# Kernel optimization log

Measured on AMD Instinct MI355X. Metric: run time of the kernel, lower is better.

The kernel has to match this reference:

```python
import jax, jax.numpy as jnp
import numpy as np

N, E, C1, E2, C2, B = 30000, 400000, 15000, 100000, 7500, 16
FV, FE, NC = 6, 3, 10


def _lin(k, i, o):
    kw, kb = jax.random.split(k)
    s = 1.0 / np.sqrt(i)
    w = jax.random.uniform(kw, (i, o), jnp.float32, -s, s)
    b = jax.random.uniform(kb, (o,), jnp.float32, -s, s)
    return w, b


def setup_inputs() -> dict:
    key = jax.random.key(0)
    ks = jax.random.split(key, 20)
    inp = {}
    inp["x"] = jax.random.normal(ks[0], (N, FV), jnp.float32)
    inp["edge_attr"] = jax.random.uniform(ks[1], (E, FE), jnp.float32)
    inp["pos"] = jax.random.uniform(ks[2], (N, 3), jnp.float32)
    inp["edge_index"] = jax.random.randint(ks[3], (2, E), 0, N)
    inp["batch"] = jnp.sort(jax.random.randint(ks[4], (N,), 0, B))
    inp["cluster1"] = jax.random.randint(ks[5], (N,), 0, C1)
    inp["edge_index2"] = jax.random.randint(ks[6], (2, E2), 0, C1)
    inp["cluster2"] = jax.random.randint(ks[7], (C1,), 0, C2)
    inp["w1a"], inp["b1a"] = _lin(ks[8], FE, 25)
    inp["w1b"], inp["b1b"] = _lin(ks[9], 25, 32 * FV)
    inp["root1"] = jax.random.normal(ks[10], (FV, 32), jnp.float32) / np.sqrt(FV)
    inp["bias1"] = jnp.zeros((32,), jnp.float32)
    inp["w2a"], inp["b2a"] = _lin(ks[11], 3, 25)
    inp["w2b"], inp["b2b"] = _lin(ks[12], 25, 32 * 64)
    inp["root2"] = jax.random.normal(ks[13], (32, 64), jnp.float32) / np.sqrt(32)
    inp["bias2"] = jnp.zeros((64,), jnp.float32)
    inp["fc1_w"], inp["fc1_b"] = _lin(ks[14], 64, 128)
    inp["fc2_w"], inp["fc2_b"] = _lin(ks[15], 128, NC)
    return inp


def _seg_mean(v, idx, n):
    s = jax.ops.segment_sum(v, idx, num_segments=n)
    c = jax.ops.segment_sum(jnp.ones(idx.shape, v.dtype), idx, num_segments=n)
    return s / jnp.maximum(c, 1.0)[:, None]


def _seg_max(v, idx, n):
    m = jax.ops.segment_max(v, idx, num_segments=n)
    return jnp.where(jnp.isfinite(m), m, 0.0)  # empty clusters -> 0


def _nnconv(x, src, dst, ea, wa, ba, wb, bb, root, bias, n, ci, co):
    # per-edge weight matrix from edge MLP: [E, ci, co]
    W = (jax.nn.relu(ea @ wa + ba) @ wb + bb).reshape(-1, ci, co)
    msg = jnp.einsum('ei,eio->eo', x[src], W)  # gather + per-edge matmul
    return _seg_mean(msg, dst, n) + x @ root + bias  # scatter-mean + root


def _cartesian(pos, src, dst):
    cart = pos[src] - pos[dst]
    return cart / (2.0 * jnp.max(jnp.abs(cart))) + 0.5  # T.Cartesian(norm=True)


def reference(x, edge_attr, pos, w1a, b1a, w1b, b1b, root1, bias1,
              w2a, b2a, w2b, b2b, root2, bias2, fc1_w, fc1_b, fc2_w, fc2_b,
              edge_index, batch, cluster1, edge_index2, cluster2):
    src1, dst1 = edge_index[0], edge_index[1]
    x1 = jax.nn.elu(_nnconv(x, src1, dst1, edge_attr, w1a, b1a, w1b, b1b,
                            root1, bias1, N, FV, 32))
    # max_pool with precomputed graclus cluster assignment
    xp = _seg_max(x1, cluster1, C1)
    posp = _seg_mean(pos, cluster1, C1)
    batchp = jnp.maximum(jax.ops.segment_max(batch, cluster1, num_segments=C1), 0)
    src2, dst2 = edge_index2[0], edge_index2[1]
    ea2 = _cartesian(posp, src2, dst2)
    x2 = jax.nn.elu(_nnconv(xp, src2, dst2, ea2, w2a, b2a, w2b, b2b,
                            root2, bias2, C1, 32, 64))
    # max_pool_x with second cluster assignment
    x3 = _seg_max(x2, cluster2, C2)
    batch2 = jnp.maximum(jax.ops.segment_max(batchp, cluster2, num_segments=C2), 0)
    g = _seg_mean(x3, batch2, B)  # global mean pool -> [B, 64]
    h = jax.nn.elu(g @ fc1_w + fc1_b)
    # dropout is identity in eval mode
    return jax.nn.log_softmax(h @ fc2_w + fc2_b, axis=1)
```

## Files before the change

kernel.cpp:

```cpp
#include <hip/hip_runtime.h>
#include <hip/hip_bf16.h>

#define Nn 30000
#define Ee 400000
#define C1n 15000
#define E2n 100000
#define C2n 7500
#define Bb 16

#define OFF_SUM1   0
#define OFF_CNT1   960000
#define OFF_XPKEY  990000
#define OFF_POSSUM 1470000
#define OFF_CNTC1  1515000
#define OFF_BPMAX  1530000
#define OFF_SUM2   1545000
#define OFF_CNT2   2505000
#define OFF_X3KEY  2520000
#define OFF_B2MAX  3000000
#define OFF_GSUM   3007500
#define OFF_GCNT   3008524
#define OFF_MAXABS 3008540
#define ZERO_ELEMS 3008544
#define OFF_X1     3008544
#define OFF_XP     3968544
#define OFF_POSP   4448544
#define OFF_CART   4493544
#define OFF_H2     4793544
#define OFF_T2     7293544
#define OFF_X2     19773544

typedef __attribute__((ext_vector_type(8))) short short8;
typedef __attribute__((ext_vector_type(4))) float f32x4;

__device__ __forceinline__ unsigned fkey(float f) {
    unsigned u = __float_as_uint(f);
    return (u >> 31) ? ~u : (u | 0x80000000u);
}
__device__ __forceinline__ float funkey(unsigned k) {
    unsigned u = (k >> 31) ? (k ^ 0x80000000u) : ~k;
    return __uint_as_float(u);
}
__device__ __forceinline__ float elu(float a) { return a > 0.f ? a : expm1f(a); }

__device__ __forceinline__ unsigned short f2bf(float f) {
    unsigned u = __float_as_uint(f);
    unsigned lsb = (u >> 16) & 1u;
    u += 0x7fffu + lsb;
    return (unsigned short)(u >> 16);
}
__device__ __forceinline__ float bf2f(unsigned short s) {
    return __uint_as_float(((unsigned)s) << 16);
}

__global__ __launch_bounds__(256, 4) void conv1_mfma(
    const float* __restrict__ x, const float* __restrict__ ea,
    const int* __restrict__ ei,
    const float* __restrict__ w1a, const float* __restrict__ b1a,
    const float* __restrict__ w1b, const float* __restrict__ b1b,
    float* __restrict__ sum1, float* __restrict__ cnt1) {
    const int lane = threadIdx.x & 63;
    const int m = lane & 15;
    const int q = lane >> 4;

    short8 Bf[6][2];
#pragma unroll
    for (int s = 0; s < 6; ++s) {
#pragma unroll
        for (int h = 0; h < 2; ++h) {
            short8 pk;
#pragma unroll
            for (int j = 0; j < 8; ++j) {
                const int u = s * 8 + j;
                const int t = u / 6, i = u % 6;
                float w = 0.f;
                if (t < 7) {
                    int k = q + 4 * t;
                    int col = h * 16 + m;
                    if (k < 25)       w = w1b[k * 192 + i * 32 + col];
                    else if (k == 25) w = b1b[i * 32 + col];
                }
                pk[j] = (short)f2bf(w);
            }
            Bf[s][h] = pk;
        }
    }

    const int wid = (blockIdx.x * blockDim.x + threadIdx.x) >> 6;
    const int nw = (gridDim.x * blockDim.x) >> 6;
    for (int tile = wid; tile < Ee / 16; tile += nw) {
        const int e0 = tile * 16;
        const int e = e0 + m;
        const int src = ei[e];
        const float ea0 = ea[e * 3], ea1 = ea[e * 3 + 1], ea2 = ea[e * 3 + 2];
        float xs[6];
#pragma unroll
        for (int i = 0; i < 6; ++i) xs[i] = x[src * 6 + i];

        float hh[8];
#pragma unroll
        for (int t = 0; t < 6; ++t) {
            int k = q + 4 * t;
            float a = b1a[k] + ea0 * w1a[k] + ea1 * w1a[25 + k] + ea2 * w1a[50 + k];
            hh[t] = fmaxf(a, 0.f);
        }
        {
            if (q == 0) {
                float a = b1a[24] + ea0 * w1a[24] + ea1 * w1a[49] + ea2 * w1a[74];
                hh[6] = fmaxf(a, 0.f);
            } else hh[6] = (q == 1) ? 1.f : 0.f;
        }
        hh[7] = 0.f;

        f32x4 acc0 = {0.f, 0.f, 0.f, 0.f}, acc1 = {0.f, 0.f, 0.f, 0.f};
#pragma unroll
        for (int s = 0; s < 6; ++s) {
            short8 av;
#pragma unroll
            for (int j = 0; j < 8; ++j) {
                const int u = s * 8 + j;
                av[j] = (short)f2bf(hh[u / 6] * xs[u % 6]);
            }
            acc0 = __builtin_amdgcn_mfma_f32_16x16x32_bf16(av, Bf[s][0], acc0, 0, 0, 0);
            acc1 = __builtin_amdgcn_mfma_f32_16x16x32_bf16(av, Bf[s][1], acc1, 0, 0, 0);
        }

#pragma unroll
        for (int r = 0; r < 4; ++r) {
            const int row = q * 4 + r;
            const int dstr = ei[Ee + e0 + row];
            atomicAdd(&sum1[dstr * 32 + m], acc0[r]);
            atomicAdd(&sum1[dstr * 32 + 16 + m], acc1[r]);
        }
        if (q == 0) {
            const int dstm = ei[Ee + e0 + m];
            atomicAdd(&cnt1[dstm], 1.f);
        }
    }
}

__global__ void x1_kernel(const float* __restrict__ sum1, const float* __restrict__ cnt1,
                          const float* __restrict__ x, const float* __restrict__ root1,
                          const float* __restrict__ bias1, float* __restrict__ x1) {
    int t = blockIdx.x * 256 + threadIdx.x;
    if (t >= Nn * 32) return;
    int n = t >> 5, o = t & 31;
    float a = sum1[t] / fmaxf(cnt1[n], 1.f) + bias1[o];
#pragma unroll
    for (int i = 0; i < 6; ++i) a += x[n * 6 + i] * root1[i * 32 + o];
    x1[t] = elu(a);
}

__global__ void pool1_kernel(const float* __restrict__ x1, const float* __restrict__ pos,
                             const int* __restrict__ batch, const int* __restrict__ cluster1,
                             unsigned* __restrict__ xpkey, float* __restrict__ possum,
                             float* __restrict__ cntc1, int* __restrict__ bpmax) {
    int t = blockIdx.x * 256 + threadIdx.x;
    if (t >= Nn * 32) return;
    int n = t >> 5, o = t & 31;
    int c = cluster1[n];
    atomicMax(&xpkey[c * 32 + o], fkey(x1[t]));
    if (o == 0) {
#pragma unroll
        for (int j = 0; j < 3; ++j) atomicAdd(&possum[c * 3 + j], pos[n * 3 + j]);
        atomicAdd(&cntc1[c], 1.f);
        atomicMax(&bpmax[c], batch[n]);
    }
}

__global__ void pool1_final(const unsigned* __restrict__ xpkey, const float* __restrict__ possum,
                            const float* __restrict__ cntc1, float* __restrict__ xp,
                            float* __restrict__ posp) {
    int t = blockIdx.x * 256 + threadIdx.x;
    if (t >= C1n * 32) return;
    int c = t >> 5, o = t & 31;
    unsigned k = xpkey[t];
    xp[t] = k ? funkey(k) : 0.f;
    if (o < 3) posp[c * 3 + o] = possum[c * 3 + o] / fmaxf(cntc1[c], 1.f);
}

__global__ void cart_kernel(const float* __restrict__ posp, const int* __restrict__ ei2,
                            float* __restrict__ cart, unsigned* __restrict__ maxabs) {
    int e = blockIdx.x * 256 + threadIdx.x;
    float mx = 0.f;
    if (e < E2n) {
        int s = ei2[e], d = ei2[E2n + e];
#pragma unroll
        for (int j = 0; j < 3; ++j) {
            float cv = posp[s * 3 + j] - posp[d * 3 + j];
            cart[e * 3 + j] = cv;
            mx = fmaxf(mx, fabsf(cv));
        }
    }
#pragma unroll
    for (int off = 32; off > 0; off >>= 1) mx = fmaxf(mx, __shfl_xor(mx, off));
    if ((threadIdx.x & 63) == 0) atomicMax(maxabs, __float_as_uint(mx));
}

__global__ void h2_kernel(const float* __restrict__ cart, const unsigned* __restrict__ maxabs,
                          const float* __restrict__ w2a, const float* __restrict__ b2a,
                          float* __restrict__ h2) {
    int t = blockIdx.x * 256 + threadIdx.x;
    if (t >= E2n * 25) return;
    int e = t / 25, k = t % 25;
    float inv = 0.5f / __uint_as_float(maxabs[0]);
    float a = b2a[k];
#pragma unroll
    for (int j = 0; j < 3; ++j) a += (cart[e * 3 + j] * inv + 0.5f) * w2a[j * 25 + k];
    h2[t] = fmaxf(a, 0.f);
}

__global__ __launch_bounds__(256) void t2_gemm(const float* __restrict__ xp,
                                               const float* __restrict__ w2b,
                                               const float* __restrict__ b2b,
                                               unsigned short* __restrict__ T2) {
    __shared__ float As[256 * 36];
    __shared__ float Bs[32][68];
    const int bm = blockIdx.x * 256;
    const int bn = blockIdx.y * 64;
    const int t = threadIdx.x;
#pragma unroll
    for (int r = 0; r < 8; ++r) {
        int qd = t + r * 256;
        int row = qd >> 3, i4 = (qd & 7) * 4;
        int n = bm + row;
        float4 v = make_float4(0.f, 0.f, 0.f, 0.f);
        if (n < C1n) v = *reinterpret_cast<const float4*>(&xp[n * 32 + i4]);
        *reinterpret_cast<float4*>(&As[row * 36 + i4]) = v;
    }
#pragma unroll
    for (int r = 0; r < 8; ++r) {
        int idx = t + r * 256;
        int i = idx >> 6, nn = idx & 63;
        int col = bn + nn;
        float v;
        if (col < 1600) { int k = col >> 6, o = col & 63; v = w2b[k * 2048 + i * 64 + o]; }
        else            { v = b2b[i * 64 + (col & 63)]; }
        Bs[i][nn] = v;
    }
    __syncthreads();
    const int tn4 = (t & 15) * 4;
    const int tr = t >> 4;
    for (int it = 0; it < 8; ++it) {
        int r0 = it * 32 + tr, r1 = r0 + 16;
        float a0[32], a1[32];
#pragma unroll
        for (int qd = 0; qd < 8; ++qd) {
            *reinterpret_cast<float4*>(&a0[qd * 4]) = *reinterpret_cast<const float4*>(&As[r0 * 36 + qd * 4]);
            *reinterpret_cast<float4*>(&a1[qd * 4]) = *reinterpret_cast<const float4*>(&As[r1 * 36 + qd * 4]);
        }
        float acc0[4] = {0.f, 0.f, 0.f, 0.f}, acc1[4] = {0.f, 0.f, 0.f, 0.f};
#pragma unroll
        for (int k = 0; k < 32; ++k) {
            float4 bv = *reinterpret_cast<const float4*>(&Bs[k][tn4]);
            acc0[0] += a0[k] * bv.x; acc0[1] += a0[k] * bv.y;
            acc0[2] += a0[k] * bv.z; acc0[3] += a0[k] * bv.w;
            acc1[0] += a1[k] * bv.x; acc1[1] += a1[k] * bv.y;
            acc1[2] += a1[k] * bv.z; acc1[3] += a1[k] * bv.w;
        }
        int row0 = bm + r0, row1 = bm + r1;
        if (row0 < C1n) {
            union { unsigned short us[4]; uint2 v; } pk;
            pk.us[0] = f2bf(acc0[0]); pk.us[1] = f2bf(acc0[1]);
            pk.us[2] = f2bf(acc0[2]); pk.us[3] = f2bf(acc0[3]);
            *reinterpret_cast<uint2*>(&T2[(size_t)row0 * 1664 + bn + tn4]) = pk.v;
        }
        if (row1 < C1n) {
            union { unsigned short us[4]; uint2 v; } pk;
            pk.us[0] = f2bf(acc1[0]); pk.us[1] = f2bf(acc1[1]);
            pk.us[2] = f2bf(acc1[2]); pk.us[3] = f2bf(acc1[3]);
            *reinterpret_cast<uint2*>(&T2[(size_t)row1 * 1664 + bn + tn4]) = pk.v;
        }
    }
}

__global__ void conv2_msg(const unsigned short* __restrict__ T2, const float* __restrict__ h2,
                          const int* __restrict__ ei2, float* __restrict__ sum2,
                          float* __restrict__ cnt2) {
    int t = blockIdx.x * 256 + threadIdx.x;
    if (t >= E2n * 64) return;
    int e = t >> 6, o = t & 63;
    int src = ei2[e], dst = ei2[E2n + e];
    const unsigned short* Trow = T2 + (size_t)src * 1664;
    float acc = bf2f(Trow[25 * 64 + o]);
#pragma unroll
    for (int k = 0; k < 25; ++k) acc += h2[e * 25 + k] * bf2f(Trow[k * 64 + o]);
    atomicAdd(&sum2[dst * 64 + o], acc);
    if (o == 0) atomicAdd(&cnt2[dst], 1.f);
}

__global__ void x2_kernel(const float* __restrict__ sum2, const float* __restrict__ cnt2,
                          const float* __restrict__ xp, const float* __restrict__ root2,
                          const float* __restrict__ bias2, float* __restrict__ x2) {
    int t = blockIdx.x * 256 + threadIdx.x;
    if (t >= C1n * 64) return;
    int c = t >> 6, o = t & 63;
    float a = sum2[t] / fmaxf(cnt2[c], 1.f) + bias2[o];
#pragma unroll
    for (int i = 0; i < 32; ++i) a += xp[c * 32 + i] * root2[i * 64 + o];
    x2[t] = elu(a);
}

__global__ void pool2_kernel(const float* __restrict__ x2, const int* __restrict__ cluster2,
                             const int* __restrict__ bpmax, unsigned* __restrict__ x3key,
                             int* __restrict__ b2max) {
    int t = blockIdx.x * 256 + threadIdx.x;
    if (t >= C1n * 64) return;
    int c = t >> 6, o = t & 63;
    int c2 = cluster2[c];
    atomicMax(&x3key[c2 * 64 + o], fkey(x2[t]));
    if (o == 0) atomicMax(&b2max[c2], bpmax[c]);
}

__global__ __launch_bounds__(256) void gacc_kernel(
    const unsigned* __restrict__ x3key, const int* __restrict__ b2max,
    float* __restrict__ gsum, float* __restrict__ gcnt) {
    __shared__ float ls[Bb * 64];
    __shared__ float lc[Bb];
    const int t = threadIdx.x;
    for (int i = t; i < Bb * 64; i += 256) ls[i] = 0.f;
    if (t < Bb) lc[t] = 0.f;
    __syncthreads();
    const int o = t & 63;
    const int cs = t >> 6;
    for (int c = blockIdx.x * 4 + cs; c < C2n; c += gridDim.x * 4) {
        int b = b2max[c];
        unsigned k = x3key[c * 64 + o];
        float v = k ? funkey(k) : 0.f;
        atomicAdd(&ls[b * 64 + o], v);
        if (o == 0) atomicAdd(&lc[b], 1.f);
    }
    __syncthreads();
    for (int i = t; i < Bb * 64; i += 256) {
        float v = ls[i];
        if (v != 0.f) atomicAdd(&gsum[i], v);
    }
    if (t < Bb) {
        float v = lc[t];
        if (v != 0.f) atomicAdd(&gcnt[t], v);
    }
}

__global__ void head_kernel(const float* __restrict__ gsum, const float* __restrict__ gcnt,
                            const float* __restrict__ fc1w, const float* __restrict__ fc1b,
                            const float* __restrict__ fc2w, const float* __restrict__ fc2b,
                            float* __restrict__ out) {
    __shared__ float g[16 * 64];
    __shared__ float hb[16 * 128];
    __shared__ float lg[16 * 10];
    __shared__ float rowm[16];
    int t = threadIdx.x;
    for (int idx = t; idx < 16 * 64; idx += 256) {
        int b = idx >> 6;
        g[idx] = gsum[idx] / fmaxf(gcnt[b], 1.f);
    }
    __syncthreads();
    for (int idx = t; idx < 16 * 128; idx += 256) {
        int b = idx >> 7, j = idx & 127;
        float a = fc1b[j];
        for (int i = 0; i < 64; ++i) a += g[b * 64 + i] * fc1w[i * 128 + j];
        hb[idx] = elu(a);
    }
    __syncthreads();
    for (int idx = t; idx < 160; idx += 256) {
        int b = idx / 10, c = idx % 10;
        float a = fc2b[c];
        for (int i = 0; i < 128; ++i) a += hb[b * 128 + i] * fc2w[i * 10 + c];
        lg[idx] = a;
    }
    __syncthreads();
    if (t < 16) {
        float m = -1e30f;
        for (int c = 0; c < 10; ++c) m = fmaxf(m, lg[t * 10 + c]);
        float s = 0.f;
        for (int c = 0; c < 10; ++c) s += expf(lg[t * 10 + c] - m);
        rowm[t] = m + logf(s);
    }
    __syncthreads();
    for (int idx = t; idx < 160; idx += 256) out[idx] = lg[idx] - rowm[idx / 10];
}

extern "C" void kernel_launch(void* const* d_in, const int* in_sizes, int n_in,
                              void* d_out, int out_size, void* d_ws, size_t ws_size,
                              hipStream_t stream) {
    const float* x     = (const float*)d_in[0];
    const float* ea    = (const float*)d_in[1];
    const float* pos   = (const float*)d_in[2];
    const int*   ei    = (const int*)d_in[3];
    const int*   batch = (const int*)d_in[4];
    const int*   cl1   = (const int*)d_in[5];
    const int*   ei2   = (const int*)d_in[6];
    const int*   cl2   = (const int*)d_in[7];
    const float* w1a   = (const float*)d_in[8];
    const float* b1a   = (const float*)d_in[9];
    const float* w1b   = (const float*)d_in[10];
    const float* b1b   = (const float*)d_in[11];
    const float* root1 = (const float*)d_in[12];
    const float* bias1 = (const float*)d_in[13];
    const float* w2a   = (const float*)d_in[14];
    const float* b2a   = (const float*)d_in[15];
    const float* w2b   = (const float*)d_in[16];
    const float* b2b   = (const float*)d_in[17];
    const float* root2 = (const float*)d_in[18];
    const float* bias2 = (const float*)d_in[19];
    const float* fc1w  = (const float*)d_in[20];
    const float* fc1b  = (const float*)d_in[21];
    const float* fc2w  = (const float*)d_in[22];
    const float* fc2b  = (const float*)d_in[23];
    float* out = (float*)d_out;

    float* ws = (float*)d_ws;
    float*    sum1   = ws + OFF_SUM1;
    float*    cnt1   = ws + OFF_CNT1;
    unsigned* xpkey  = (unsigned*)(ws + OFF_XPKEY);
    float*    possum = ws + OFF_POSSUM;
    float*    cntc1  = ws + OFF_CNTC1;
    int*      bpmax  = (int*)(ws + OFF_BPMAX);
    float*    sum2   = ws + OFF_SUM2;
    float*    cnt2   = ws + OFF_CNT2;
    unsigned* x3key  = (unsigned*)(ws + OFF_X3KEY);
    int*      b2max  = (int*)(ws + OFF_B2MAX);
    float*    gsum   = ws + OFF_GSUM;
    float*    gcnt   = ws + OFF_GCNT;
    unsigned* maxabs = (unsigned*)(ws + OFF_MAXABS);
    float*    x1     = ws + OFF_X1;
    float*    xp     = ws + OFF_XP;
    float*    posp   = ws + OFF_POSP;
    float*    cart   = ws + OFF_CART;
    float*    h2     = ws + OFF_H2;
    unsigned short* T2 = (unsigned short*)(ws + OFF_T2);
    float*    x2     = ws + OFF_X2;

    hipMemsetAsync(ws, 0, (size_t)ZERO_ELEMS * 4, stream);

    conv1_mfma<<<1024, 256, 0, stream>>>(x, ea, ei, w1a, b1a, w1b, b1b, sum1, cnt1);
    x1_kernel<<<(Nn * 32 + 255) / 256, 256, 0, stream>>>(sum1, cnt1, x, root1, bias1, x1);
    pool1_kernel<<<(Nn * 32 + 255) / 256, 256, 0, stream>>>(x1, pos, batch, cl1, xpkey, possum, cntc1, bpmax);
    pool1_final<<<(C1n * 32 + 255) / 256, 256, 0, stream>>>(xpkey, possum, cntc1, xp, posp);
    cart_kernel<<<(E2n + 255) / 256, 256, 0, stream>>>(posp, ei2, cart, maxabs);
    h2_kernel<<<(E2n * 25 + 255) / 256, 256, 0, stream>>>(cart, maxabs, w2a, b2a, h2);
    dim3 tgrid((C1n + 255) / 256, 26);
    t2_gemm<<<tgrid, 256, 0, stream>>>(xp, w2b, b2b, T2);
    conv2_msg<<<(E2n * 64 + 255) / 256, 256, 0, stream>>>(T2, h2, ei2, sum2, cnt2);
    x2_kernel<<<(C1n * 64 + 255) / 256, 256, 0, stream>>>(sum2, cnt2, xp, root2, bias2, x2);
    pool2_kernel<<<(C1n * 64 + 255) / 256, 256, 0, stream>>>(x2, cl2, bpmax, x3key, b2max);
    gacc_kernel<<<32, 256, 0, stream>>>(x3key, b2max, gsum, gcnt);
    head_kernel<<<1, 256, 0, stream>>>(gsum, gcnt, fc1w, fc1b, fc2w, fc2b, out);
}
```

Measured before the change: 352.9 us.

## Aggregate per-destination edge features via CSR then apply NNConv weights once per node

Builds CSR edge lists by destination (histogram, scan, scatter) and uses linearity of NNConv to aggregate h⊗x outer products per destination node before multiplying by the weight matrix. Each layer then runs one MFMA GEMM per node that also folds in root weights, bias, ELU and the cluster max-pool. This replaces per-edge float atomics and the large T2 intermediate with per-node gathers. In exchange it adds CSR-building kernels and serial per-node loops that can be imbalanced on high-degree nodes.

After: 416.2 us. 17.9% more time.

```diff
diff --git a/kernel.cpp b/kernel.cpp
--- a/kernel.cpp
+++ b/kernel.cpp
@@ -8,27 +8,31 @@
 #define C2n 7500
 #define Bb 16
 
-#define OFF_SUM1   0
-#define OFF_CNT1   960000
-#define OFF_XPKEY  990000
-#define OFF_POSSUM 1470000
-#define OFF_CNTC1  1515000
-#define OFF_BPMAX  1530000
-#define OFF_SUM2   1545000
-#define OFF_CNT2   2505000
-#define OFF_X3KEY  2520000
-#define OFF_B2MAX  3000000
-#define OFF_GSUM   3007500
-#define OFF_GCNT   3008524
-#define OFF_MAXABS 3008540
-#define ZERO_ELEMS 3008544
-#define OFF_X1     3008544
-#define OFF_XP     3968544
-#define OFF_POSP   4448544
-#define OFF_CART   4493544
-#define OFF_H2     4793544
-#define OFF_T2     7293544
-#define OFF_X2     19773544
+#define OFF_XPKEY   0
+#define OFF_POSSUM  480000
+#define OFF_CNTC1   525000
+#define OFF_BPMAX   540000
+#define OFF_X3KEY   555000
+#define OFF_B2MAX   1035000
+#define OFF_GSUM    1042500
+#define OFF_GCNT    1043524
+#define OFF_MAXABS  1043540
+#define OFF_DEG1    1043544
+#define OFF_FILL1   1073544
+#define OFF_DEG2    1103544
+#define OFF_FILL2   1118544
+#define ZERO_ELEMS  1133544
+#define OFF_RP1     1133544
+#define OFF_RP2     1163548
+#define OFF_EIDS1   1178552
+#define OFF_EIDS2   1578552
+#define OFF_POSP    1678552
+#define OFF_CART    1723552
+#define OFF_XP      2023552
+#define OFF_W1T     2503552
+#define OFF_W2T     2506624
+#define OFF_G1      2535296
+#define OFF_G2      5415296
 
 typedef __attribute__((ext_vector_type(8))) short short8;
 typedef __attribute__((ext_vector_type(4))) float f32x4;
@@ -49,122 +53,183 @@
     u += 0x7fffu + lsb;
     return (unsigned short)(u >> 16);
 }
-__device__ __forceinline__ float bf2f(unsigned short s) {
-    return __uint_as_float(((unsigned)s) << 16);
-}
-
-__global__ __launch_bounds__(256, 4) void conv1_mfma(
-    const float* __restrict__ x, const float* __restrict__ ea,
-    const int* __restrict__ ei,
+
+__global__ void hist_kernel(const int* __restrict__ ei, const int* __restrict__ ei2,
+                            unsigned* __restrict__ deg1, unsigned* __restrict__ deg2) {
+    int t = blockIdx.x * 256 + threadIdx.x;
+    if (t < Ee) {
+        atomicAdd(&deg1[ei[Ee + t]], 1u);
+    } else if (t < Ee + E2n) {
+        int e = t - Ee;
+        atomicAdd(&deg2[ei2[E2n + e]], 1u);
+    }
+}
+
+__global__ __launch_bounds__(1024) void scan_both(
+    const unsigned* __restrict__ deg1, unsigned* __restrict__ rp1,
+    const unsigned* __restrict__ deg2, unsigned* __restrict__ rp2) {
+    const unsigned* deg; unsigned* rp; int n;
+    if (blockIdx.x == 0) { deg = deg1; rp = rp1; n = Nn; }
+    else                 { deg = deg2; rp = rp2; n = C1n; }
+    __shared__ unsigned ps[1024];
+    const int t = threadIdx.x;
+    const int chunk = (n + 1023) / 1024;
+    const int lo = t * chunk;
+    const int hi = (lo + chunk < n) ? lo + chunk : n;
+    unsigned s = 0;
+    for (int i = lo; i < hi; ++i) s += deg[i];
+    ps[t] = s;
+    __syncthreads();
+    for (int off = 1; off < 1024; off <<= 1) {
+        unsigned v = (t >= off) ? ps[t - off] : 0u;
+        __syncthreads();
+        ps[t] += v;
+        __syncthreads();
+    }
+    unsigned run = (t > 0) ? ps[t - 1] : 0u;
+    if (t == 0) rp[0] = 0u;
+    for (int i = lo; i < hi; ++i) { run += deg[i]; rp[i + 1] = run; }
+}
+
+__global__ void scatter_kernel(const int* __restrict__ ei, const int* __restrict__ ei2,
+                               const unsigned* __restrict__ rp1, unsigned* __restrict__ fill1,
+                               unsigned* __restrict__ eids1,
+                               const unsigned* __restrict__ rp2, unsigned* __restrict__ fill2,
+                               unsigned* __restrict__ eids2) {
+    int t = blockIdx.x * 256 + threadIdx.x;
+    if (t < Ee) {
+        int d = ei[Ee + t];
+        unsigned p = atomicAdd(&fill1[d], 1u);
+        eids1[rp1[d] + p] = (unsigned)t;
+    } else if (t < Ee + E2n) {
+        int e = t - Ee;
+        int d = ei2[E2n + e];
+        unsigned p = atomicAdd(&fill2[d], 1u);
+        eids2[rp2[d] + p] = (unsigned)e;
+    }
+}
+
+__global__ void wt_kernel(const float* __restrict__ w1b, const float* __restrict__ b1b,
+                          const float* __restrict__ root1, const float* __restrict__ bias1,
+                          const float* __restrict__ w2b, const float* __restrict__ b2b,
+                          const float* __restrict__ root2, const float* __restrict__ bias2,
+                          unsigned short* __restrict__ W1T, unsigned short* __restrict__ W2T) {
+    int t = blockIdx.x * 256 + threadIdx.x;
+    if (t < 32 * 192) {
+        int col = t / 192, p = t % 192;
+        float v;
+        if (p < 150)       { int k = p / 6, i = p % 6; v = w1b[k * 192 + i * 32 + col]; }
+        else if (p < 156)  { int i = p - 150; v = b1b[i * 32 + col]; }
+        else if (p < 162)  { v = root1[(p - 156) * 32 + col]; }
+        else if (p == 162) { v = bias1[col]; }
+        else v = 0.f;
+        W1T[t] = f2bf(v);
+    } else {
+        int u = t - 32 * 192;
+        if (u < 64 * 896) {
+            int col = u / 896, p = u % 896;
+            float v;
+            if (p < 800)       { int k = p / 32, i = p % 32; v = w2b[k * 2048 + i * 64 + col]; }
+            else if (p < 832)  { int i = p - 800; v = b2b[i * 64 + col]; }
+            else if (p < 864)  { v = root2[(p - 832) * 64 + col]; }
+            else if (p == 864) { v = bias2[col]; }
+            else v = 0.f;
+            W2T[u] = f2bf(v);
+        }
+    }
+}
+
+__global__ __launch_bounds__(256, 8) void g1_kernel(
+    const float* __restrict__ x, const float* __restrict__ ea, const int* __restrict__ ei,
+    const unsigned* __restrict__ rp1, const unsigned* __restrict__ eids1,
     const float* __restrict__ w1a, const float* __restrict__ b1a,
-    const float* __restrict__ w1b, const float* __restrict__ b1b,
-    float* __restrict__ sum1, float* __restrict__ cnt1) {
-    const int lane = threadIdx.x & 63;
-    const int m = lane & 15;
-    const int q = lane >> 4;
-
-    short8 Bf[6][2];
-#pragma unroll
-    for (int s = 0; s < 6; ++s) {
-#pragma unroll
-        for (int h = 0; h < 2; ++h) {
-            short8 pk;
-#pragma unroll
-            for (int j = 0; j < 8; ++j) {
-                const int u = s * 8 + j;
-                const int t = u / 6, i = u % 6;
-                float w = 0.f;
-                if (t < 7) {
-                    int k = q + 4 * t;
-                    int col = h * 16 + m;
-                    if (k < 25)       w = w1b[k * 192 + i * 32 + col];
-                    else if (k == 25) w = b1b[i * 32 + col];
-                }
-                pk[j] = (short)f2bf(w);
-            }
-            Bf[s][h] = pk;
-        }
-    }
-
+    unsigned short* __restrict__ G1) {
+    const int l = threadIdx.x & 63;
+    int k_[3], i_[3];
+#pragma unroll
+    for (int r = 0; r < 3; ++r) { int j = r * 64 + l; k_[r] = j / 6; i_[r] = j % 6; }
+    float wa0 = 0.f, wa1 = 0.f, wa2 = 0.f, ba0 = 0.f;
+    if (l < 25) { wa0 = w1a[l]; wa1 = w1a[25 + l]; wa2 = w1a[50 + l]; ba0 = b1a[l]; }
     const int wid = (blockIdx.x * blockDim.x + threadIdx.x) >> 6;
     const int nw = (gridDim.x * blockDim.x) >> 6;
-    for (int tile = wid; tile < Ee / 16; tile += nw) {
-        const int e0 = tile * 16;
-        const int e = e0 + m;
-        const int src = ei[e];
-        const float ea0 = ea[e * 3], ea1 = ea[e * 3 + 1], ea2 = ea[e * 3 + 2];
-        float xs[6];
-#pragma unroll
-        for (int i = 0; i < 6; ++i) xs[i] = x[src * 6 + i];
-
-        float hh[8];
-#pragma unroll
-        for (int t = 0; t < 6; ++t) {
-            int k = q + 4 * t;
-            float a = b1a[k] + ea0 * w1a[k] + ea1 * w1a[25 + k] + ea2 * w1a[50 + k];
-            hh[t] = fmaxf(a, 0.f);
-        }
-        {
-            if (q == 0) {
-                float a = b1a[24] + ea0 * w1a[24] + ea1 * w1a[49] + ea2 * w1a[74];
-                hh[6] = fmaxf(a, 0.f);
-            } else hh[6] = (q == 1) ? 1.f : 0.f;
-        }
-        hh[7] = 0.f;
-
+    for (int d = wid; d < Nn; d += nw) {
+        const unsigned e0 = rp1[d], e1 = rp1[d + 1];
+        float acc[3] = {0.f, 0.f, 0.f};
+        if (e0 < e1) {
+            int eid = (int)eids1[e0];
+            float c0 = ea[eid * 3], c1 = ea[eid * 3 + 1], c2 = ea[eid * 3 + 2];
+            int src = ei[eid];
+            for (unsigned p = e0; p < e1; ++p) {
+                const float pc0 = c0, pc1 = c1, pc2 = c2;
+                const int psrc = src;
+                if (p + 1 < e1) {
+                    int en = (int)eids1[p + 1];
+                    c0 = ea[en * 3]; c1 = ea[en * 3 + 1]; c2 = ea[en * 3 + 2];
+                    src = ei[en];
+                }
+                float xa = x[psrc * 6 + i_[0]];
+                float xb = x[psrc * 6 + i_[1]];
+                float xc = x[psrc * 6 + i_[2]];
+                float a = ba0 + pc0 * wa0 + pc1 * wa1 + pc2 * wa2;
+                float hown = (l == 25) ? 1.f : fmaxf(a, 0.f);
+                acc[0] += __shfl(hown, k_[0], 64) * xa;
+                acc[1] += __shfl(hown, k_[1], 64) * xb;
+                acc[2] += __shfl(hown, k_[2], 64) * xc;
+            }
+        }
+        const float dinv = 1.f / fmaxf((float)(e1 - e0), 1.f);
+        const size_t gb = (size_t)d * 192;
+#pragma unroll
+        for (int r = 0; r < 3; ++r) {
+            int j = r * 64 + l;
+            float val;
+            if (j < 156)       val = acc[r] * dinv;
+            else if (j < 162)  val = x[d * 6 + (j - 156)];
+            else if (j == 162) val = 1.f;
+            else               val = 0.f;
+            G1[gb + j] = f2bf(val);
+        }
+    }
+}
+
+__global__ __launch_bounds__(256, 4) void conv1_fused(
+    const unsigned short* __restrict__ G1, const unsigned short* __restrict__ W1T,
+    const float* __restrict__ pos, const int* __restrict__ batch, const int* __restrict__ cl1,
+    unsigned* __restrict__ xpkey, float* __restrict__ possum,
+    float* __restrict__ cntc1, int* __restrict__ bpmax) {
+    const int lane = threadIdx.x & 63;
+    const int m = lane & 15, q = lane >> 4;
+    short8 Bf[6][2];
+#pragma unroll
+    for (int s = 0; s < 6; ++s)
+#pragma unroll
+        for (int h = 0; h < 2; ++h)
+            Bf[s][h] = *reinterpret_cast<const short8*>(&W1T[(h * 16 + m) * 192 + s * 32 + q * 8]);
+    const int wid = (blockIdx.x * blockDim.x + threadIdx.x) >> 6;
+    const int nw = (gridDim.x * blockDim.x) >> 6;
+    for (int tile = wid; tile < Nn / 16; tile += nw) {
+        const int base = tile * 16;
         f32x4 acc0 = {0.f, 0.f, 0.f, 0.f}, acc1 = {0.f, 0.f, 0.f, 0.f};
 #pragma unroll
         for (int s = 0; s < 6; ++s) {
-            short8 av;
-#pragma unroll
-            for (int j = 0; j < 8; ++j) {
-                const int u = s * 8 + j;
-                av[j] = (short)f2bf(hh[u / 6] * xs[u % 6]);
-            }
+            short8 av = *reinterpret_cast<const short8*>(&G1[(size_t)(base + m) * 192 + s * 32 + q * 8]);
             acc0 = __builtin_amdgcn_mfma_f32_16x16x32_bf16(av, Bf[s][0], acc0, 0, 0, 0);
             acc1 = __builtin_amdgcn_mfma_f32_16x16x32_bf16(av, Bf[s][1], acc1, 0, 0, 0);
         }
-
 #pragma unroll
         for (int r = 0; r < 4; ++r) {
-            const int row = q * 4 + r;
-            const int dstr = ei[Ee + e0 + row];
-            atomicAdd(&sum1[dstr * 32 + m], acc0[r]);
-            atomicAdd(&sum1[dstr * 32 + 16 + m], acc1[r]);
-        }
-        if (q == 0) {
-            const int dstm = ei[Ee + e0 + m];
-            atomicAdd(&cnt1[dstm], 1.f);
-        }
-    }
-}
-
-__global__ void x1_kernel(const float* __restrict__ sum1, const float* __restrict__ cnt1,
-                          const float* __restrict__ x, const float* __restrict__ root1,
-                          const float* __restrict__ bias1, float* __restrict__ x1) {
-    int t = blockIdx.x * 256 + threadIdx.x;
-    if (t >= Nn * 32) return;
-    int n = t >> 5, o = t & 31;
-    float a = sum1[t] / fmaxf(cnt1[n], 1.f) + bias1[o];
-#pragma unroll
-    for (int i = 0; i < 6; ++i) a += x[n * 6 + i] * root1[i * 32 + o];
-    x1[t] = elu(a);
-}
-
-__global__ void pool1_kernel(const float* __restrict__ x1, const float* __restrict__ pos,
-                             const int* __restrict__ batch, const int* __restrict__ cluster1,
-                             unsigned* __restrict__ xpkey, float* __restrict__ possum,
-                             float* __restrict__ cntc1, int* __restrict__ bpmax) {
-    int t = blockIdx.x * 256 + threadIdx.x;
-    if (t >= Nn * 32) return;
-    int n = t >> 5, o = t & 31;
-    int c = cluster1[n];
-    atomicMax(&xpkey[c * 32 + o], fkey(x1[t]));
-    if (o == 0) {
-#pragma unroll
-        for (int j = 0; j < 3; ++j) atomicAdd(&possum[c * 3 + j], pos[n * 3 + j]);
-        atomicAdd(&cntc1[c], 1.f);
-        atomicMax(&bpmax[c], batch[n]);
+            const int row = base + q * 4 + r;
+            const int c = cl1[row];
+            float v0 = elu(acc0[r]), v1 = elu(acc1[r]);
+            atomicMax(&xpkey[c * 32 + m], fkey(v0));
+            atomicMax(&xpkey[c * 32 + 16 + m], fkey(v1));
+            if (m == 0) {
+#pragma unroll
+                for (int j = 0; j < 3; ++j) atomicAdd(&possum[c * 3 + j], pos[row * 3 + j]);
+                atomicAdd(&cntc1[c], 1.f);
+                atomicMax(&bpmax[c], batch[row]);
+            }
+        }
     }
 }
 
@@ -197,119 +262,93 @@
     if ((threadIdx.x & 63) == 0) atomicMax(maxabs, __float_as_uint(mx));
 }
 
-__global__ void h2_kernel(const float* __restrict__ cart, const unsigned* __restrict__ maxabs,
-                          const float* __restrict__ w2a, const float* __restrict__ b2a,
-                          float* __restrict__ h2) {
-    int t = blockIdx.x * 256 + threadIdx.x;
-    if (t >= E2n * 25) return;
-    int e = t / 25, k = t % 25;
-    float inv = 0.5f / __uint_as_float(maxabs[0]);
-    float a = b2a[k];
-#pragma unroll
-    for (int j = 0; j < 3; ++j) a += (cart[e * 3 + j] * inv + 0.5f) * w2a[j * 25 + k];
-    h2[t] = fmaxf(a, 0.f);
-}
-
-__global__ __launch_bounds__(256) void t2_gemm(const float* __restrict__ xp,
-                                               const float* __restrict__ w2b,
-                                               const float* __restrict__ b2b,
-                                               unsigned short* __restrict__ T2) {
-    __shared__ float As[256 * 36];
-    __shared__ float Bs[32][68];
-    const int bm = blockIdx.x * 256;
-    const int bn = blockIdx.y * 64;
-    const int t = threadIdx.x;
-#pragma unroll
-    for (int r = 0; r < 8; ++r) {
-        int qd = t + r * 256;
-        int row = qd >> 3, i4 = (qd & 7) * 4;
-        int n = bm + row;
-        float4 v = make_float4(0.f, 0.f, 0.f, 0.f);
-        if (n < C1n) v = *reinterpret_cast<const float4*>(&xp[n * 32 + i4]);
-        *reinterpret_cast<float4*>(&As[row * 36 + i4]) = v;
-    }
-#pragma unroll
-    for (int r = 0; r < 8; ++r) {
-        int idx = t + r * 256;
-        int i = idx >> 6, nn = idx & 63;
-        int col = bn + nn;
-        float v;
-        if (col < 1600) { int k = col >> 6, o = col & 63; v = w2b[k * 2048 + i * 64 + o]; }
-        else            { v = b2b[i * 64 + (col & 63)]; }
-        Bs[i][nn] = v;
-    }
-    __syncthreads();
-    const int tn4 = (t & 15) * 4;
-    const int tr = t >> 4;
-    for (int it = 0; it < 8; ++it) {
-        int r0 = it * 32 + tr, r1 = r0 + 16;
-        float a0[32], a1[32];
-#pragma unroll
-        for (int qd = 0; qd < 8; ++qd) {
-            *reinterpret_cast<float4*>(&a0[qd * 4]) = *reinterpret_cast<const float4*>(&As[r0 * 36 + qd * 4]);
-            *reinterpret_cast<float4*>(&a1[qd * 4]) = *reinterpret_cast<const float4*>(&As[r1 * 36 + qd * 4]);
-        }
-        float acc0[4] = {0.f, 0.f, 0.f, 0.f}, acc1[4] = {0.f, 0.f, 0.f, 0.f};
-#pragma unroll
-        for (int k = 0; k < 32; ++k) {
-            float4 bv = *reinterpret_cast<const float4*>(&Bs[k][tn4]);
-            acc0[0] += a0[k] * bv.x; acc0[1] += a0[k] * bv.y;
-            acc0[2] += a0[k] * bv.z; acc0[3] += a0[k] * bv.w;
-            acc1[0] += a1[k] * bv.x; acc1[1] += a1[k] * bv.y;
-            acc1[2] += a1[k] * bv.z; acc1[3] += a1[k] * bv.w;
-        }
-        int row0 = bm + r0, row1 = bm + r1;
-        if (row0 < C1n) {
-            union { unsigned short us[4]; uint2 v; } pk;
-            pk.us[0] = f2bf(acc0[0]); pk.us[1] = f2bf(acc0[1]);
-            pk.us[2] = f2bf(acc0[2]); pk.us[3] = f2bf(acc0[3]);
-            *reinterpret_cast<uint2*>(&T2[(size_t)row0 * 1664 + bn + tn4]) = pk.v;
-        }
-        if (row1 < C1n) {
-            union { unsigned short us[4]; uint2 v; } pk;
-            pk.us[0] = f2bf(acc1[0]); pk.us[1] = f2bf(acc1[1]);
-            pk.us[2] = f2bf(acc1[2]); pk.us[3] = f2bf(acc1[3]);
-            *reinterpret_cast<uint2*>(&T2[(size_t)row1 * 1664 + bn + tn4]) = pk.v;
-        }
-    }
-}
-
-__global__ void conv2_msg(const unsigned short* __restrict__ T2, const float* __restrict__ h2,
-                          const int* __restrict__ ei2, float* __restrict__ sum2,
-                          float* __restrict__ cnt2) {
-    int t = blockIdx.x * 256 + threadIdx.x;
-    if (t >= E2n * 64) return;
-    int e = t >> 6, o = t & 63;
-    int src = ei2[e], dst = ei2[E2n + e];
-    const unsigned short* Trow = T2 + (size_t)src * 1664;
-    float acc = bf2f(Trow[25 * 64 + o]);
-#pragma unroll
-    for (int k = 0; k < 25; ++k) acc += h2[e * 25 + k] * bf2f(Trow[k * 64 + o]);
-    atomicAdd(&sum2[dst * 64 + o], acc);
-    if (o == 0) atomicAdd(&cnt2[dst], 1.f);
-}
-
-__global__ void x2_kernel(const float* __restrict__ sum2, const float* __restrict__ cnt2,
-                          const float* __restrict__ xp, const float* __restrict__ root2,
-                          const float* __restrict__ bias2, float* __restrict__ x2) {
-    int t = blockIdx.x * 256 + threadIdx.x;
-    if (t >= C1n * 64) return;
-    int c = t >> 6, o = t & 63;
-    float a = sum2[t] / fmaxf(cnt2[c], 1.f) + bias2[o];
-#pragma unroll
-    for (int i = 0; i < 32; ++i) a += xp[c * 32 + i] * root2[i * 64 + o];
-    x2[t] = elu(a);
-}
-
-__global__ void pool2_kernel(const float* __restrict__ x2, const int* __restrict__ cluster2,
-                             const int* __restrict__ bpmax, unsigned* __restrict__ x3key,
-                             int* __restrict__ b2max) {
-    int t = blockIdx.x * 256 + threadIdx.x;
-    if (t >= C1n * 64) return;
-    int c = t >> 6, o = t & 63;
-    int c2 = cluster2[c];
-    atomicMax(&x3key[c2 * 64 + o], fkey(x2[t]));
-    if (o == 0) atomicMax(&b2max[c2], bpmax[c]);
+__global__ __launch_bounds__(256, 4) void g2_kernel(
+    const float* __restrict__ xp, const float* __restrict__ cart,
+    const unsigned* __restrict__ maxabs, const int* __restrict__ ei2,
+    const unsigned* __restrict__ rp2, const unsigned* __restrict__ eids2,
+    const float* __restrict__ w2a, const float* __restrict__ b2a,
+    unsigned short* __restrict__ G2) {
+    const int l = threadIdx.x & 63;
+    const int i = l & 31, hp = l >> 5;
+    float wa0 = 0.f, wa1 = 0.f, wa2 = 0.f, ba0 = 0.f;
+    if (l < 25) { wa0 = w2a[l]; wa1 = w2a[25 + l]; wa2 = w2a[50 + l]; ba0 = b2a[l]; }
+    const float inv = 0.5f / __uint_as_float(maxabs[0]);
+    const int wid = (blockIdx.x * blockDim.x + threadIdx.x) >> 6;
+    const int nw = (gridDim.x * blockDim.x) >> 6;
+    for (int d = wid; d < C1n; d += nw) {
+        const unsigned e0 = rp2[d], e1 = rp2[d + 1];
+        float acc[13];
+#pragma unroll
+        for (int r = 0; r < 13; ++r) acc[r] = 0.f;
+        if (e0 < e1) {
+            int eid = (int)eids2[e0];
+            float c0 = cart[eid * 3], c1 = cart[eid * 3 + 1], c2 = cart[eid * 3 + 2];
+            int src = ei2[eid];
+            for (unsigned p = e0; p < e1; ++p) {
+                const float pc0 = c0, pc1 = c1, pc2 = c2;
+                const int psrc = src;
+                if (p + 1 < e1) {
+                    int en = (int)eids2[p + 1];
+                    c0 = cart[en * 3]; c1 = cart[en * 3 + 1]; c2 = cart[en * 3 + 2];
+                    src = ei2[en];
+                }
+                float xv = xp[psrc * 32 + i];
+                float a = ba0 + (pc0 * inv + 0.5f) * wa0 + (pc1 * inv + 0.5f) * wa1
+                              + (pc2 * inv + 0.5f) * wa2;
+                float hown = (l == 25) ? 1.f : fmaxf(a, 0.f);
+#pragma unroll
+                for (int r = 0; r < 13; ++r)
+                    acc[r] += __shfl(hown, 2 * r + hp, 64) * xv;
+            }
+        }
+        const float dinv = 1.f / fmaxf((float)(e1 - e0), 1.f);
+        const size_t gb = (size_t)d * 896;
+#pragma unroll
+        for (int r = 0; r < 13; ++r) G2[gb + r * 64 + l] = f2bf(acc[r] * dinv);
+        float tail = (l < 32) ? xp[d * 32 + l] : (l == 32 ? 1.f : 0.f);
+        G2[gb + 832 + l] = f2bf(tail);
+    }
+}
+
+__global__ __launch_bounds__(256, 4) void conv2_fused(
+    const unsigned short* __restrict__ G2, const unsigned short* __restrict__ W2T,
+    const int* __restrict__ cl2, const int* __restrict__ bpmax,
+    unsigned* __restrict__ x3key, int* __restrict__ b2max) {
+    const int lane = threadIdx.x & 63;
+    const int m = lane & 15, q = lane >> 4;
+    const int wid = (blockIdx.x * blockDim.x + threadIdx.x) >> 6;
+    const int nw = (gridDim.x * blockDim.x) >> 6;
+    const int ntiles = (C1n + 15) / 16;
+    for (int tile = wid; tile < ntiles; tile += nw) {
+        const int base = tile * 16;
+        int arow = base + m;
+        if (arow >= C1n) arow = C1n - 1;
+        f32x4 acc[4];
+#pragma unroll
+        for (int h = 0; h < 4; ++h) acc[h] = (f32x4){0.f, 0.f, 0.f, 0.f};
+#pragma unroll 4
+        for (int s = 0; s < 28; ++s) {
+            short8 av = *reinterpret_cast<const short8*>(&G2[(size_t)arow * 896 + s * 32 + q * 8]);
+#pragma unroll
+            for (int h = 0; h < 4; ++h) {
+                short8 bv = *reinterpret_cast<const short8*>(&W2T[(h * 16 + m) * 896 + s * 32 + q * 8]);
+                acc[h] = __builtin_amdgcn_mfma_f32_16x16x32_bf16(av, bv, acc[h], 0, 0, 0);
+            }
+        }
+#pragma unroll
+        for (int r = 0; r < 4; ++r) {
+            const int row = base + q * 4 + r;
+            if (row < C1n) {
+                const int c2 = cl2[row];
+#pragma unroll
+                for (int h = 0; h < 4; ++h) {
+                    float v = elu(acc[h][r]);
+                    atomicMax(&x3key[c2 * 64 + h * 16 + m], fkey(v));
+                }
+                if (m == 0) atomicMax(&b2max[c2], bpmax[row]);
+            }
+        }
+    }
 }
 
 __global__ __launch_bounds__(256) void gacc_kernel(
@@ -410,40 +449,44 @@
     float* out = (float*)d_out;
 
     float* ws = (float*)d_ws;
-    float*    sum1   = ws + OFF_SUM1;
-    float*    cnt1   = ws + OFF_CNT1;
     unsigned* xpkey  = (unsigned*)(ws + OFF_XPKEY);
     float*    possum = ws + OFF_POSSUM;
     float*    cntc1  = ws + OFF_CNTC1;
     int*      bpmax  = (int*)(ws + OFF_BPMAX);
-    float*    sum2   = ws + OFF_SUM2;
-    float*    cnt2   = ws + OFF_CNT2;
     unsigned* x3key  = (unsigned*)(ws + OFF_X3KEY);
     int*      b2max  = (int*)(ws + OFF_B2MAX);
     float*    gsum   = ws + OFF_GSUM;
     float*    gcnt   = ws + OFF_GCNT;
     unsigned* maxabs = (unsigned*)(ws + OFF_MAXABS);
-    float*    x1     = ws + OFF_X1;
-    float*    xp     = ws + OFF_XP;
+    unsigned* deg1   = (unsigned*)(ws + OFF_DEG1);
+    unsigned* fill1  = (unsigned*)(ws + OFF_FILL1);
+    unsigned* deg2   = (unsigned*)(ws + OFF_DEG2);
+    unsigned* fill2  = (unsigned*)(ws + OFF_FILL2);
+    unsigned* rp1    = (unsigned*)(ws + OFF_RP1);
+    unsigned* rp2    = (unsigned*)(ws + OFF_RP2);
+    unsigned* eids1  = (unsigned*)(ws + OFF_EIDS1);
+    unsigned* eids2  = (unsigned*)(ws + OFF_EIDS2);
     float*    posp   = ws + OFF_POSP;
     float*    cart   = ws + OFF_CART;
-    float*    h2     = ws + OFF_H2;
-    unsigned short* T2 = (unsigned short*)(ws + OFF_T2);
-    float*    x2     = ws + OFF_X2;
+    float*    xp     = ws + OFF_XP;
+    unsigned short* W1T = (unsigned short*)(ws + OFF_W1T);
+    unsigned short* W2T = (unsigned short*)(ws + OFF_W2T);
+    unsigned short* G1  = (unsigned short*)(ws + OFF_G1);
+    unsigned short* G2  = (unsigned short*)(ws + OFF_G2);
 
     hipMemsetAsync(ws, 0, (size_t)ZERO_ELEMS * 4, stream);
 
-    conv1_mfma<<<1024, 256, 0, stream>>>(x, ea, ei, w1a, b1a, w1b, b1b, sum1, cnt1);
-    x1_kernel<<<(Nn * 32 + 255) / 256, 256, 0, stream>>>(sum1, cnt1, x, root1, bias1, x1);
-    pool1_kernel<<<(Nn * 32 + 255) / 256, 256, 0, stream>>>(x1, pos, batch, cl1, xpkey, possum, cntc1, bpmax);
+    wt_kernel<<<248, 256, 0, stream>>>(w1b, b1b, root1, bias1, w2b, b2b, root2, bias2, W1T, W2T);
+    hist_kernel<<<(Ee + E2n + 255) / 256, 256, 0, stream>>>(ei, ei2, deg1, deg2);
+    scan_both<<<2, 1024, 0, stream>>>(deg1, rp1, deg2, rp2);
+    scatter_kernel<<<(Ee + E2n + 255) / 256, 256, 0, stream>>>(ei, ei2, rp1, fill1, eids1,
+                                                               rp2, fill2, eids2);
+    g1_kernel<<<2048, 256, 0, stream>>>(x, ea, ei, rp1, eids1, w1a, b1a, G1);
+    conv1_fused<<<469, 256, 0, stream>>>(G1, W1T, pos, batch, cl1, xpkey, possum, cntc1, bpmax);
     pool1_final<<<(C1n * 32 + 255) / 256, 256, 0, stream>>>(xpkey, possum, cntc1, xp, posp);
     cart_kernel<<<(E2n + 255) / 256, 256, 0, stream>>>(posp, ei2, cart, maxabs);
-    h2_kernel<<<(E2n * 25 + 255) / 256, 256, 0, stream>>>(cart, maxabs, w2a, b2a, h2);
-    dim3 tgrid((C1n + 255) / 256, 26);
-    t2_gemm<<<tgrid, 256, 0, stream>>>(xp, w2b, b2b, T2);
-    conv2_msg<<<(E2n * 64 + 255) / 256, 256, 0, stream>>>(T2, h2, ei2, sum2, cnt2);
-    x2_kernel<<<(C1n * 64 + 255) / 256, 256, 0, stream>>>(sum2, cnt2, xp, root2, bias2, x2);
-    pool2_kernel<<<(C1n * 64 + 255) / 256, 256, 0, stream>>>(x2, cl2, bpmax, x3key, b2max);
+    g2_kernel<<<1024, 256, 0, stream>>>(xp, cart, maxabs, ei2, rp2, eids2, w2a, b2a, G2);
+    conv2_fused<<<235, 256, 0, stream>>>(G2, W2T, cl2, bpmax, x3key, b2max);
     gacc_kernel<<<32, 256, 0, stream>>>(x3key, b2max, gsum, gcnt);
     head_kernel<<<1, 256, 0, stream>>>(gsum, gcnt, fc1w, fc1b, fc2w, fc2b, out);
 }
```
